# Performance work log

Hardware: AMD Instinct MI355X
Metric: run time of the kernel (lower is better)

Reference implementation:

```python
import jax, jax.numpy as jnp
import numpy as np

LN_EPS = 1e-5


def _layer_norm(x, scale, bias):
    mu = jnp.mean(x, axis=-1, keepdims=True)
    var = jnp.mean(jnp.square(x - mu), axis=-1, keepdims=True)
    return (x - mu) * jax.lax.rsqrt(var + LN_EPS) * scale + bias


def setup_inputs() -> dict:
    key = jax.random.key(0)
    B, N, C_Z, C_H = 1, 512, 128, 128
    ks = jax.random.split(key, 8)
    s = 1.0 / np.sqrt(C_Z)
    inp = {
        "z": jax.random.normal(ks[0], (B, N, N, C_Z), dtype=jnp.float32),
        "mask": jnp.ones((B, N, N), dtype=jnp.float32),
        # gated / plain projections from c_z -> c_hidden
        "w_a_p": jax.random.normal(ks[1], (C_Z, C_H), dtype=jnp.float32) * s,
        "b_a_p": jnp.zeros((C_H,), dtype=jnp.float32),
        "w_a_g": jnp.zeros((C_Z, C_H), dtype=jnp.float32),  # gating init: zeros, bias ones
        "b_a_g": jnp.ones((C_H,), dtype=jnp.float32),
        "w_b_p": jax.random.normal(ks[2], (C_Z, C_H), dtype=jnp.float32) * s,
        "b_b_p": jnp.zeros((C_H,), dtype=jnp.float32),
        "w_b_g": jnp.zeros((C_Z, C_H), dtype=jnp.float32),
        "b_b_g": jnp.ones((C_H,), dtype=jnp.float32),
        # output gate c_z -> c_z (gating init)
        "w_g": jnp.zeros((C_Z, C_Z), dtype=jnp.float32),
        "b_g": jnp.ones((C_Z,), dtype=jnp.float32),
        # final projection c_hidden -> c_z ('final' init: zeros; use small randn for a nontrivial test)
        "w_z": jax.random.normal(ks[3], (C_H, C_Z), dtype=jnp.float32) * (1.0 / np.sqrt(C_H)),
        "b_z": jnp.zeros((C_Z,), dtype=jnp.float32),
        "ln_in_scale": jnp.ones((C_Z,), dtype=jnp.float32),
        "ln_in_bias": jnp.zeros((C_Z,), dtype=jnp.float32),
        "ln_out_scale": jnp.ones((C_H,), dtype=jnp.float32),
        "ln_out_bias": jnp.zeros((C_H,), dtype=jnp.float32),
    }
    return inp


def reference(z, mask, w_a_p, b_a_p, w_a_g, b_a_g, w_b_p, b_b_p, w_b_g, b_b_g,
              w_g, b_g, w_z, b_z, ln_in_scale, ln_in_bias, ln_out_scale, ln_out_bias):
    # tmu_type == 'outgoing'
    z = _layer_norm(z, ln_in_scale, ln_in_bias)          # [B,N,N,Cz]
    m = mask[..., None]                                   # [B,N,N,1]
    a = jax.nn.sigmoid(z @ w_a_g + b_a_g) * m * (z @ w_a_p + b_a_p)  # [B,N,N,Ch]
    b = jax.nn.sigmoid(z @ w_b_g + b_b_g) * m * (z @ w_b_p + b_b_p)  # [B,N,N,Ch]
    # outgoing: p[b,i,j,c] = sum_k a[b,i,k,c] * b[b,j,k,c]
    x = jnp.einsum("bikc,bjkc->bijc", a, b)              # [B,N,N,Ch]
    x = _layer_norm(x, ln_out_scale, ln_out_bias)
    x = x @ w_z + b_z                                    # [B,N,N,Cz]
    g = jax.nn.sigmoid(z @ w_g + b_g)                    # [B,N,N,Cz]
    return x * g
```

## Files before the change

kernel.cpp:

```cpp
#include <hip/hip_runtime.h>

typedef __attribute__((ext_vector_type(8))) short short8;
typedef __attribute__((ext_vector_type(4))) short short4v;
typedef __attribute__((ext_vector_type(4))) float float4v;
typedef __attribute__((ext_vector_type(2))) unsigned int uint2v;

#define NDIM 512
#define NN (NDIM*NDIM)
#define CD 128

__device__ __forceinline__ unsigned short f2b(float f) {
  union { float f; unsigned u; } v; v.f = f;
  unsigned r = v.u + 0x7FFFu + ((v.u >> 16) & 1u);
  return (unsigned short)(r >> 16);
}
__device__ __forceinline__ float b2f(unsigned short h) {
  union { unsigned u; float f; } v; v.u = ((unsigned)h) << 16; return v.f;
}
__device__ __forceinline__ float sigmoidf_(float x) { return 1.f / (1.f + __expf(-x)); }
__device__ __forceinline__ unsigned pk2(float a, float b) {
  return (unsigned)f2b(a) | ((unsigned)f2b(b) << 16);
}
__device__ __forceinline__ float4v mfma16(short8 a, short8 b, float4v c) {
  return __builtin_amdgcn_mfma_f32_16x16x32_bf16(a, b, c, 0, 0, 0);
}
__device__ __forceinline__ void gl_lds16(const short* g, short* l) {
  __builtin_amdgcn_global_load_lds(
      (const __attribute__((address_space(1))) unsigned int*)g,
      (__attribute__((address_space(3))) unsigned int*)l, 16, 0, 0);
}

__device__ __forceinline__ short8 fragr(const short* buf, int row, int j) {
  return *(const short8*)(buf + row * 128 + ((j ^ (row & 15)) << 3));
}

__device__ __forceinline__ void stageW(const short* wslot, short* sW, int t) {
#pragma unroll
  for (int i = 0; i < 8; ++i) {
    int U = i * 256 + t;
    int row = U >> 4, u = U & 15;
    gl_lds16(wslot + row * 128 + ((u ^ (row & 15)) << 3), sW + U * 8);
  }
}

__global__ __launch_bounds__(256) void kPrepW(
    const float* __restrict__ w0, const float* __restrict__ w1,
    const float* __restrict__ w2, const float* __restrict__ w3,
    const float* __restrict__ w4, short* __restrict__ wt)
{
  const int wi = blockIdx.y;
  const float* W = wi==0 ? w0 : wi==1 ? w1 : wi==2 ? w2 : wi==3 ? w3 : w4;
  const int e = blockIdx.x * 256 + threadIdx.x;
  const int k = e >> 7, n = e & 127;
  wt[wi * 16384 + n * 128 + k] = (short)f2b(W[k * CD + n]);
}

__global__ __launch_bounds__(256, 2) void kProj(
    const float* __restrict__ z, const float* __restrict__ mask,
    const short* __restrict__ wT,
    const float* __restrict__ b_a_p, const float* __restrict__ b_a_g,
    const float* __restrict__ b_b_p, const float* __restrict__ b_b_g,
    const float* __restrict__ b_g,
    const float* __restrict__ ln_s, const float* __restrict__ ln_b,
    short* __restrict__ a_t, short* __restrict__ b_t, short* __restrict__ g_out)
{
  __shared__ short zln[128 * 128];
  __shared__ short sW[128 * 128];
  const int t = threadIdx.x;
  const int r0 = blockIdx.x * 128;
  const int w = t >> 6, l = t & 63, lr = l & 15, lg = l >> 4;

  stageW(wT + 1 * 16384, sW, t);

#pragma unroll
  for (int h = 0; h < 2; ++h) {
    const int row = h * 64 + (t >> 2), q = t & 3;
    const float* zp = z + (size_t)(r0 + row) * CD + q * 32;
    float x[32];
#pragma unroll
    for (int i = 0; i < 8; ++i) {
      float4v v = *(const float4v*)(zp + i * 4);
#pragma unroll
      for (int e = 0; e < 4; ++e) x[i*4+e] = v[e];
    }
    float s = 0.f;
#pragma unroll
    for (int i = 0; i < 32; ++i) s += x[i];
    s += __shfl_xor(s, 1, 64);
    s += __shfl_xor(s, 2, 64);
    const float mu = s * (1.f/128.f);
    float vs = 0.f;
#pragma unroll
    for (int i = 0; i < 32; ++i) { float d = x[i]-mu; vs += d*d; }
    vs += __shfl_xor(vs, 1, 64);
    vs += __shfl_xor(vs, 2, 64);
    const float rstd = rsqrtf(vs * (1.f/128.f) + 1e-5f);
#pragma unroll
    for (int i = 0; i < 32; ++i) {
      int c = q*32 + i;
      float y = (x[i]-mu)*rstd*ln_s[c] + ln_b[c];
      zln[row*128 + (((c>>3) ^ (row & 15)) << 3) + (c & 7)] = (short)f2b(y);
    }
  }

  float bga[8], bpa[8], bgb[8], bpb[8];
#pragma unroll
  for (int cf = 0; cf < 8; ++cf) {
    bga[cf] = b_a_g[cf*16+lr]; bpa[cf] = b_a_p[cf*16+lr];
    bgb[cf] = b_b_g[cf*16+lr]; bpb[cf] = b_b_p[cf*16+lr];
  }
  float mrow[2][4];
#pragma unroll
  for (int g = 0; g < 2; ++g)
#pragma unroll
    for (int jj = 0; jj < 4; ++jj)
      mrow[g][jj] = mask[r0 + w*32 + g*16 + lg*4 + jj];

  __syncthreads();

  short8 af[2][4];
#pragma unroll
  for (int g = 0; g < 2; ++g)
#pragma unroll
    for (int ks = 0; ks < 4; ++ks)
      af[g][ks] = fragr(zln, w*32 + g*16 + lr, ks*4 + lg);

  float4v accA[2][8], accB[2][8];
  float sg[2][8][4];

#define ZERO_ACC(A) do { _Pragma("unroll") for (int g_=0;g_<2;++g_) \
  _Pragma("unroll") for (int c_=0;c_<8;++c_) A[g_][c_] = (float4v){0.f,0.f,0.f,0.f}; } while(0)

#define WPASS(A) do { ZERO_ACC(A);                                         \
  _Pragma("unroll") for (int ks_=0; ks_<4; ++ks_)                          \
    _Pragma("unroll") for (int cf_=0; cf_<8; ++cf_) {                      \
      short8 wf_ = fragr(sW, cf_*16 + lr, ks_*4 + lg);                     \
      _Pragma("unroll") for (int g_=0; g_<2; ++g_)                         \
        A[g_][cf_] = mfma16(af[g_][ks_], wf_, A[g_][cf_]);                 \
    } } while(0)

#define SIGPASS(BG) do { _Pragma("unroll") for (int g_=0;g_<2;++g_)        \
  _Pragma("unroll") for (int cf_=0;cf_<8;++cf_)                            \
    _Pragma("unroll") for (int j_=0;j_<4;++j_)                             \
      sg[g_][cf_][j_] = sigmoidf_(accA[g_][cf_][j_] + BG[cf_]) * mrow[g_][j_]; } while(0)

#define STORE_AB(DST, BP) do { _Pragma("unroll") for (int g_=0;g_<2;++g_)  \
  _Pragma("unroll") for (int cf_=0;cf_<8;++cf_) {                          \
    float v0_ = sg[g_][cf_][0] * (accB[g_][cf_][0] + BP[cf_]);             \
    float v1_ = sg[g_][cf_][1] * (accB[g_][cf_][1] + BP[cf_]);             \
    float v2_ = sg[g_][cf_][2] * (accB[g_][cf_][2] + BP[cf_]);             \
    float v3_ = sg[g_][cf_][3] * (accB[g_][cf_][3] + BP[cf_]);             \
    uint2v pv_ = { pk2(v0_, v1_), pk2(v2_, v3_) };                         \
    *(uint2v*)(DST + (size_t)(cf_*16+lr)*NN + r0 + w*32 + g_*16 + lg*4) = pv_; \
  } } while(0)

  WPASS(accA);
  SIGPASS(bga);
  __syncthreads();
  stageW(wT + 0 * 16384, sW, t);
  __syncthreads();
  WPASS(accB);
  __syncthreads();
  stageW(wT + 3 * 16384, sW, t);
  STORE_AB(a_t, bpa);
  __syncthreads();
  WPASS(accA);
  SIGPASS(bgb);
  __syncthreads();
  stageW(wT + 2 * 16384, sW, t);
  __syncthreads();
  WPASS(accB);
  __syncthreads();
  stageW(wT + 4 * 16384, sW, t);
  STORE_AB(b_t, bpb);
  __syncthreads();
  {
    float4v accG[2][8];
    ZERO_ACC(accG);
#pragma unroll
    for (int ks = 0; ks < 4; ++ks)
#pragma unroll
      for (int cf = 0; cf < 8; ++cf) {
        short8 wf = fragr(sW, cf*16 + lr, ks*4 + lg);
#pragma unroll
        for (int g = 0; g < 2; ++g)
          accG[g][cf] = mfma16(wf, af[g][ks], accG[g][cf]);
      }
#pragma unroll
    for (int g = 0; g < 2; ++g)
#pragma unroll
      for (int cf = 0; cf < 8; ++cf) {
        float4v bgv = *(const float4v*)(b_g + cf*16 + lg*4);
        float v0 = sigmoidf_(accG[g][cf][0] + bgv[0]);
        float v1 = sigmoidf_(accG[g][cf][1] + bgv[1]);
        float v2 = sigmoidf_(accG[g][cf][2] + bgv[2]);
        float v3 = sigmoidf_(accG[g][cf][3] + bgv[3]);
        uint2v pv = { pk2(v0, v1), pk2(v2, v3) };
        *(uint2v*)(g_out + (size_t)(r0 + w*32 + g*16 + lr)*CD + cf*16 + lg*4) = pv;
      }
  }
}

__global__ __launch_bounds__(256, 2) void kEinsum(const short* __restrict__ a_t,
                                                  const short* __restrict__ b_t,
                                                  short* __restrict__ x_t)
{
  __shared__ short As[2][128 * 64];
  __shared__ short Bs[2][128 * 64];
  const int t = threadIdx.x;
  const int d = blockIdx.x;
  const int c = (d & 7) * 16 + (d >> 7);
  const int tile = (d >> 3) & 15;
  const int i0 = (tile >> 2) * 128;
  const int j0 = (tile & 3) * 128;
  const size_t abase = (size_t)c * NN;
  const int w = t >> 6, l = t & 63, lr = l & 15, lg = l >> 4;
  const int wr = w >> 1, wc = w & 1;

  const short* gA[4]; const short* gB[4]; int ldsU[4];
#pragma unroll
  for (int q = 0; q < 4; ++q) {
    int U = q * 256 + t;
    int row = U >> 3, u = U & 7;
    int swz = ((u ^ (row & 7)) << 3);
    gA[q] = a_t + abase + (size_t)(i0 + row) * NDIM + swz;
    gB[q] = b_t + abase + (size_t)(j0 + row) * NDIM + swz;
    ldsU[q] = U * 8;
  }

#define STAGE_E(buf, k0) do { _Pragma("unroll") for (int q_=0;q_<4;++q_) { \
    gl_lds16(gA[q_] + (k0), &As[buf][ldsU[q_]]);                           \
    gl_lds16(gB[q_] + (k0), &Bs[buf][ldsU[q_]]); } } while(0)

  float4v acc[4][4];
#pragma unroll
  for (int m = 0; m < 4; ++m)
#pragma unroll
    for (int n = 0; n < 4; ++n) acc[m][n] = (float4v){0.f,0.f,0.f,0.f};

  STAGE_E(0, 0);
  __syncthreads();
  int cur = 0;
#pragma unroll
  for (int it = 0; it < 8; ++it) {
    if (it < 7) STAGE_E(cur ^ 1, (it + 1) * 64);
    short8 afr[4][2], bfr[4][2];
#pragma unroll
    for (int m = 0; m < 4; ++m)
#pragma unroll
      for (int ks = 0; ks < 2; ++ks) {
        int row = wr*64 + m*16 + lr, j = ks*4 + lg;
        afr[m][ks] = *(const short8*)(&As[cur][row*64 + ((j ^ (row & 7)) << 3)]);
      }
#pragma unroll
    for (int n = 0; n < 4; ++n)
#pragma unroll
      for (int ks = 0; ks < 2; ++ks) {
        int row = wc*64 + n*16 + lr, j = ks*4 + lg;
        bfr[n][ks] = *(const short8*)(&Bs[cur][row*64 + ((j ^ (row & 7)) << 3)]);
      }
#pragma unroll
    for (int ks = 0; ks < 2; ++ks)
#pragma unroll
      for (int m = 0; m < 4; ++m)
#pragma unroll
        for (int n = 0; n < 4; ++n)
          acc[m][n] = mfma16(bfr[n][ks], afr[m][ks], acc[m][n]);
    __syncthreads();
    cur ^= 1;
  }
#pragma unroll
  for (int m = 0; m < 4; ++m)
#pragma unroll
    for (int n = 0; n < 4; ++n) {
      int i  = i0 + wr*64 + m*16 + lr;
      int jb = j0 + wc*64 + n*16 + lg*4;
      uint2v pv = { pk2(acc[m][n][0], acc[m][n][1]), pk2(acc[m][n][2], acc[m][n][3]) };
      *(uint2v*)(x_t + abase + (size_t)i * NDIM + jb) = pv;
    }
}

__global__ __launch_bounds__(256, 2) void kOut(
    const short* __restrict__ x_t, const short* __restrict__ g_in,
    const float* __restrict__ w_z, const float* __restrict__ b_z,
    const float* __restrict__ ln_s, const float* __restrict__ ln_b,
    float* __restrict__ out)
{
  __shared__ short xs[128 * 72];
  __shared__ short xln[64 * 128];
  __shared__ short sW[128 * 128];
  const int t = threadIdx.x;
  const int r0 = blockIdx.x * 64;
  const int w = t >> 6, l = t & 63, lr = l & 15, lg = l >> 4;

#pragma unroll
  for (int i = 0; i < 8; ++i) {
    int flat = i * 256 + t;
    int kp = flat >> 5, k = kp * 2, n4 = (flat & 31) * 4;
    float4v va = *(const float4v*)(w_z + (size_t)k * CD + n4);
    float4v vb = *(const float4v*)(w_z + (size_t)(k + 1) * CD + n4);
#pragma unroll
    for (int j = 0; j < 4; ++j) {
      int row = n4 + j;
      int addr = row * 128 + (((k >> 3) ^ (row & 15)) << 3) + (k & 7);
      *(unsigned*)(&sW[addr]) = pk2(va[j], vb[j]);
    }
  }
#pragma unroll
  for (int it = 0; it < 4; ++it) {
    int v = it * 256 + t; int cc = v >> 3; int u = v & 7;
    int up = u ^ ((cc >> 3) & 7);
    *(short8*)&xs[cc * 72 + up * 8] = *(const short8*)(x_t + (size_t)cc * NN + r0 + u * 8);
  }
  __syncthreads();
  {
    const int r = t >> 2, q = t & 3;
    float x[32];
#pragma unroll
    for (int i = 0; i < 32; ++i) {
      int c = q * 32 + i;
      x[i] = b2f((unsigned short)xs[c * 72 + (((r >> 3) ^ ((c >> 3) & 7)) << 3) + (r & 7)]);
    }
    float s = 0.f;
#pragma unroll
    for (int i = 0; i < 32; ++i) s += x[i];
    s += __shfl_xor(s, 1, 64);
    s += __shfl_xor(s, 2, 64);
    const float mu = s * (1.f/128.f);
    float vs = 0.f;
#pragma unroll
    for (int i = 0; i < 32; ++i) { float d = x[i]-mu; vs += d*d; }
    vs += __shfl_xor(vs, 1, 64);
    vs += __shfl_xor(vs, 2, 64);
    const float rstd = rsqrtf(vs * (1.f/128.f) + 1e-5f);
#pragma unroll
    for (int i = 0; i < 32; ++i) {
      int c = q*32 + i;
      float y = (x[i]-mu)*rstd*ln_s[c] + ln_b[c];
      xln[r*128 + (((c>>3) ^ (r & 15)) << 3) + (c & 7)] = (short)f2b(y);
    }
  }
  __syncthreads();
  short8 af[4];
#pragma unroll
  for (int ks = 0; ks < 4; ++ks)
    af[ks] = fragr(xln, w*16 + lr, ks*4 + lg);

  float4v acc[8];
#pragma unroll
  for (int cf = 0; cf < 8; ++cf) acc[cf] = (float4v){0.f,0.f,0.f,0.f};
#pragma unroll
  for (int ks = 0; ks < 4; ++ks)
#pragma unroll
    for (int cf = 0; cf < 8; ++cf) {
      short8 wf = fragr(sW, cf*16 + lr, ks*4 + lg);
      acc[cf] = mfma16(wf, af[ks], acc[cf]);
    }
  const int orow = r0 + w*16 + lr;
#pragma unroll
  for (int cf = 0; cf < 8; ++cf) {
    float4v bzv = *(const float4v*)(b_z + cf*16 + lg*4);
    short4v gv = *(const short4v*)(g_in + (size_t)orow * CD + cf*16 + lg*4);
    float4v o;
#pragma unroll
    for (int j = 0; j < 4; ++j)
      o[j] = (acc[cf][j] + bzv[j]) * b2f((unsigned short)gv[j]);
    *(float4v*)(out + (size_t)orow * CD + cf*16 + lg*4) = o;
  }
}

extern "C" void kernel_launch(void* const* d_in, const int* in_sizes, int n_in,
                              void* d_out, int out_size, void* d_ws, size_t ws_size,
                              hipStream_t stream) {
  (void)in_sizes; (void)n_in; (void)out_size; (void)ws_size;
  const float* z     = (const float*)d_in[0];
  const float* mask  = (const float*)d_in[1];
  const float* w_a_p = (const float*)d_in[2];
  const float* b_a_p = (const float*)d_in[3];
  const float* w_a_g = (const float*)d_in[4];
  const float* b_a_g = (const float*)d_in[5];
  const float* w_b_p = (const float*)d_in[6];
  const float* b_b_p = (const float*)d_in[7];
  const float* w_b_g = (const float*)d_in[8];
  const float* b_b_g = (const float*)d_in[9];
  const float* w_g   = (const float*)d_in[10];
  const float* b_g   = (const float*)d_in[11];
  const float* w_z   = (const float*)d_in[12];
  const float* b_z   = (const float*)d_in[13];
  const float* ln_i_s = (const float*)d_in[14];
  const float* ln_i_b = (const float*)d_in[15];
  const float* ln_o_s = (const float*)d_in[16];
  const float* ln_o_b = (const float*)d_in[17];

  short* a_t = (short*)d_ws;
  short* b_t = a_t + (size_t)CD*NN;
  short* g_s = b_t + (size_t)CD*NN;
  short* x_t = g_s + (size_t)CD*NN;
  short* wT  = x_t;

  hipLaunchKernelGGL(kPrepW, dim3(64, 5), dim3(256), 0, stream,
                     w_a_p, w_a_g, w_b_p, w_b_g, w_g, wT);
  hipLaunchKernelGGL(kProj, dim3(NN/128), dim3(256), 0, stream,
                     z, mask, wT, b_a_p, b_a_g, b_b_p, b_b_g, b_g,
                     ln_i_s, ln_i_b, a_t, b_t, g_s);
  hipLaunchKernelGGL(kEinsum, dim3(2048), dim3(256), 0, stream, a_t, b_t, x_t);
  hipLaunchKernelGGL(kOut, dim3(NN/64), dim3(256), 0, stream,
                     x_t, g_s, w_z, b_z, ln_o_s, ln_o_b, (float*)d_out);
}
```

Measured before the change: 366.0 us.

## Restructure projection kernel and stage all epilogue stores through LDS for coalescing

The projection kernel moves to 512 threads over 64 rows with double weight buffers, so gate and projection weights are staged together and fewer barriers are needed. Its channel-major a/b outputs and the g output are now written through shared memory as 16-byte coalesced stores. The einsum and output kernels also stage their epilogues through swizzled LDS before wide global stores. The einsum gains s_setprio around its MFMA block, and bf16 packing now uses a v_cvt_pk_bf16_f32 instruction. The gain is aimed at scattered narrow global writes, paid for with more LDS use and extra barriers that may reduce occupancy.

```diff
diff --git a/kernel.cpp b/kernel.cpp
--- a/kernel.cpp
+++ b/kernel.cpp
@@ -3,7 +3,6 @@
 typedef __attribute__((ext_vector_type(8))) short short8;
 typedef __attribute__((ext_vector_type(4))) short short4v;
 typedef __attribute__((ext_vector_type(4))) float float4v;
-typedef __attribute__((ext_vector_type(2))) unsigned int uint2v;
 
 #define NDIM 512
 #define NN (NDIM*NDIM)
@@ -19,7 +18,9 @@
 }
 __device__ __forceinline__ float sigmoidf_(float x) { return 1.f / (1.f + __expf(-x)); }
 __device__ __forceinline__ unsigned pk2(float a, float b) {
-  return (unsigned)f2b(a) | ((unsigned)f2b(b) << 16);
+  unsigned r;
+  asm("v_cvt_pk_bf16_f32 %0, %1, %2" : "=v"(r) : "v"(a), "v"(b));
+  return r;
 }
 __device__ __forceinline__ float4v mfma16(short8 a, short8 b, float4v c) {
   return __builtin_amdgcn_mfma_f32_16x16x32_bf16(a, b, c, 0, 0, 0);
@@ -33,14 +34,8 @@
 __device__ __forceinline__ short8 fragr(const short* buf, int row, int j) {
   return *(const short8*)(buf + row * 128 + ((j ^ (row & 15)) << 3));
 }
-
-__device__ __forceinline__ void stageW(const short* wslot, short* sW, int t) {
-#pragma unroll
-  for (int i = 0; i < 8; ++i) {
-    int U = i * 256 + t;
-    int row = U >> 4, u = U & 15;
-    gl_lds16(wslot + row * 128 + ((u ^ (row & 15)) << 3), sW + U * 8);
-  }
+__device__ __forceinline__ void stg_w(short* buf, int row, int ku, unsigned v) {
+  *(unsigned*)&buf[row * 128 + ((((ku >> 2) ^ (row & 15)) << 3) + ((ku & 3) << 1))] = v;
 }
 
 __global__ __launch_bounds__(256) void kPrepW(
@@ -55,7 +50,7 @@
   wt[wi * 16384 + n * 128 + k] = (short)f2b(W[k * CD + n]);
 }
 
-__global__ __launch_bounds__(256, 2) void kProj(
+__global__ __launch_bounds__(512, 2) void kProj(
     const float* __restrict__ z, const float* __restrict__ mask,
     const short* __restrict__ wT,
     const float* __restrict__ b_a_p, const float* __restrict__ b_a_g,
@@ -64,140 +59,158 @@
     const float* __restrict__ ln_s, const float* __restrict__ ln_b,
     short* __restrict__ a_t, short* __restrict__ b_t, short* __restrict__ g_out)
 {
-  __shared__ short zln[128 * 128];
-  __shared__ short sW[128 * 128];
+  __shared__ short zln[64 * 128];
+  __shared__ short sS[128 * 128];
+  __shared__ short wA[128 * 128];
+  __shared__ short wB[128 * 128];
   const int t = threadIdx.x;
-  const int r0 = blockIdx.x * 128;
+  const int r0 = blockIdx.x * 64;
   const int w = t >> 6, l = t & 63, lr = l & 15, lg = l >> 4;
-
-  stageW(wT + 1 * 16384, sW, t);
-
-#pragma unroll
-  for (int h = 0; h < 2; ++h) {
-    const int row = h * 64 + (t >> 2), q = t & 3;
-    const float* zp = z + (size_t)(r0 + row) * CD + q * 32;
-    float x[32];
-#pragma unroll
-    for (int i = 0; i < 8; ++i) {
+  const int wr = (w >> 1) * 16;
+  const int hc = (w & 1) * 64;
+
+#define STAGE4(BUF, SLOT) do { _Pragma("unroll") for (int i_=0;i_<4;++i_) {  \
+    int U_ = i_*512 + t; int row_ = U_ >> 4, u_ = U_ & 15;                   \
+    gl_lds16(wT + (SLOT)*16384 + row_*128 + ((u_^(row_&15))<<3), (BUF)+U_*8); } } while(0)
+
+  STAGE4(wA, 1);
+  STAGE4(wB, 0);
+
+  {
+    const int row = t >> 3, q = t & 7;
+    const float* zp = z + (size_t)(r0 + row) * CD + q * 16;
+    float x[16];
+#pragma unroll
+    for (int i = 0; i < 4; ++i) {
       float4v v = *(const float4v*)(zp + i * 4);
 #pragma unroll
       for (int e = 0; e < 4; ++e) x[i*4+e] = v[e];
     }
     float s = 0.f;
 #pragma unroll
-    for (int i = 0; i < 32; ++i) s += x[i];
+    for (int i = 0; i < 16; ++i) s += x[i];
     s += __shfl_xor(s, 1, 64);
     s += __shfl_xor(s, 2, 64);
+    s += __shfl_xor(s, 4, 64);
     const float mu = s * (1.f/128.f);
     float vs = 0.f;
 #pragma unroll
-    for (int i = 0; i < 32; ++i) { float d = x[i]-mu; vs += d*d; }
+    for (int i = 0; i < 16; ++i) { float d = x[i]-mu; vs += d*d; }
     vs += __shfl_xor(vs, 1, 64);
     vs += __shfl_xor(vs, 2, 64);
+    vs += __shfl_xor(vs, 4, 64);
     const float rstd = rsqrtf(vs * (1.f/128.f) + 1e-5f);
 #pragma unroll
-    for (int i = 0; i < 32; ++i) {
-      int c = q*32 + i;
-      float y = (x[i]-mu)*rstd*ln_s[c] + ln_b[c];
-      zln[row*128 + (((c>>3) ^ (row & 15)) << 3) + (c & 7)] = (short)f2b(y);
-    }
-  }
-
-  float bga[8], bpa[8], bgb[8], bpb[8];
-#pragma unroll
-  for (int cf = 0; cf < 8; ++cf) {
-    bga[cf] = b_a_g[cf*16+lr]; bpa[cf] = b_a_p[cf*16+lr];
-    bgb[cf] = b_b_g[cf*16+lr]; bpb[cf] = b_b_p[cf*16+lr];
-  }
-  float mrow[2][4];
-#pragma unroll
-  for (int g = 0; g < 2; ++g)
-#pragma unroll
-    for (int jj = 0; jj < 4; ++jj)
-      mrow[g][jj] = mask[r0 + w*32 + g*16 + lg*4 + jj];
-
-  __syncthreads();
-
-  short8 af[2][4];
-#pragma unroll
-  for (int g = 0; g < 2; ++g)
+    for (int i = 0; i < 16; i += 2) {
+      int c = q*16 + i;
+      float y0 = (x[i]  -mu)*rstd*ln_s[c]   + ln_b[c];
+      float y1 = (x[i+1]-mu)*rstd*ln_s[c+1] + ln_b[c+1];
+      int addr = row*128 + (((c>>3) ^ (row & 15)) << 3) + (c & 7);
+      *(unsigned*)(&zln[addr]) = pk2(y0, y1);
+    }
+  }
+
+  float bga[4], bpa[4], bgb[4], bpb[4];
+#pragma unroll
+  for (int cf = 0; cf < 4; ++cf) {
+    int ci = hc + cf*16 + lr;
+    bga[cf] = b_a_g[ci]; bpa[cf] = b_a_p[ci];
+    bgb[cf] = b_b_g[ci]; bpb[cf] = b_b_p[ci];
+  }
+  float mrow[4];
+#pragma unroll
+  for (int jj = 0; jj < 4; ++jj) mrow[jj] = mask[r0 + wr + lg*4 + jj];
+
+  __syncthreads();
+
+  short8 af[4];
+#pragma unroll
+  for (int ks = 0; ks < 4; ++ks)
+    af[ks] = fragr(zln, wr + lr, ks*4 + lg);
+
+  float4v accG[4], accB[4];
+  float sg[4][4];
+
+#define ZERO4(A) do { _Pragma("unroll") for (int c_=0;c_<4;++c_) A[c_] = (float4v){0.f,0.f,0.f,0.f}; } while(0)
+
+#define WP(ACC, BUF) do { ZERO4(ACC);                                      \
+  _Pragma("unroll") for (int ks_=0; ks_<4; ++ks_)                          \
+    _Pragma("unroll") for (int cf_=0; cf_<4; ++cf_) {                      \
+      short8 wf_ = fragr(BUF, hc + cf_*16 + lr, ks_*4 + lg);               \
+      ACC[cf_] = mfma16(af[ks_], wf_, ACC[cf_]);                           \
+    } } while(0)
+
+#define SIG4(BG) do { _Pragma("unroll") for (int cf_=0;cf_<4;++cf_)        \
+    _Pragma("unroll") for (int j_=0;j_<4;++j_)                             \
+      sg[cf_][j_] = sigmoidf_(accG[cf_][j_] + BG[cf_]) * mrow[j_]; } while(0)
+
+#define PKAB(BP) do { _Pragma("unroll") for (int cf_=0;cf_<4;++cf_) {      \
+    float v0_ = sg[cf_][0]*(accB[cf_][0]+BP[cf_]);                         \
+    float v1_ = sg[cf_][1]*(accB[cf_][1]+BP[cf_]);                         \
+    float v2_ = sg[cf_][2]*(accB[cf_][2]+BP[cf_]);                         \
+    float v3_ = sg[cf_][3]*(accB[cf_][3]+BP[cf_]);                         \
+    int ch_ = hc + cf_*16 + lr, ku_ = (wr >> 1) + lg*2;                    \
+    stg_w(sS, ch_, ku_,   pk2(v0_, v1_));                                  \
+    stg_w(sS, ch_, ku_+1, pk2(v2_, v3_)); } } while(0)
+
+#define STORE64A(DST) do { int ch_ = t >> 2;                               \
+  _Pragma("unroll") for (int i_=0;i_<2;++i_) {                             \
+    int cL_ = (t & 3)*2 + i_;                                              \
+    *(short8*)(DST + (size_t)ch_*NN + r0 + cL_*8) = fragr(sS, ch_, cL_);   \
+  } } while(0)
+
+  WP(accG, wA);
+  WP(accB, wB);
+  SIG4(bga);
+  PKAB(bpa);
+  __syncthreads();
+
+  STAGE4(wA, 3);
+  STAGE4(wB, 2);
+  STORE64A(a_t);
+  __syncthreads();
+
+  WP(accG, wA);
+  WP(accB, wB);
+  SIG4(bgb);
+  PKAB(bpb);
+  __syncthreads();
+
+  STAGE4(wA, 4);
+  STORE64A(b_t);
+  __syncthreads();
+
+  {
+    float4v accG2[4];
+    ZERO4(accG2);
 #pragma unroll
     for (int ks = 0; ks < 4; ++ks)
-      af[g][ks] = fragr(zln, w*32 + g*16 + lr, ks*4 + lg);
-
-  float4v accA[2][8], accB[2][8];
-  float sg[2][8][4];
-
-#define ZERO_ACC(A) do { _Pragma("unroll") for (int g_=0;g_<2;++g_) \
-  _Pragma("unroll") for (int c_=0;c_<8;++c_) A[g_][c_] = (float4v){0.f,0.f,0.f,0.f}; } while(0)
-
-#define WPASS(A) do { ZERO_ACC(A);                                         \
-  _Pragma("unroll") for (int ks_=0; ks_<4; ++ks_)                          \
-    _Pragma("unroll") for (int cf_=0; cf_<8; ++cf_) {                      \
-      short8 wf_ = fragr(sW, cf_*16 + lr, ks_*4 + lg);                     \
-      _Pragma("unroll") for (int g_=0; g_<2; ++g_)                         \
-        A[g_][cf_] = mfma16(af[g_][ks_], wf_, A[g_][cf_]);                 \
-    } } while(0)
-
-#define SIGPASS(BG) do { _Pragma("unroll") for (int g_=0;g_<2;++g_)        \
-  _Pragma("unroll") for (int cf_=0;cf_<8;++cf_)                            \
-    _Pragma("unroll") for (int j_=0;j_<4;++j_)                             \
-      sg[g_][cf_][j_] = sigmoidf_(accA[g_][cf_][j_] + BG[cf_]) * mrow[g_][j_]; } while(0)
-
-#define STORE_AB(DST, BP) do { _Pragma("unroll") for (int g_=0;g_<2;++g_)  \
-  _Pragma("unroll") for (int cf_=0;cf_<8;++cf_) {                          \
-    float v0_ = sg[g_][cf_][0] * (accB[g_][cf_][0] + BP[cf_]);             \
-    float v1_ = sg[g_][cf_][1] * (accB[g_][cf_][1] + BP[cf_]);             \
-    float v2_ = sg[g_][cf_][2] * (accB[g_][cf_][2] + BP[cf_]);             \
-    float v3_ = sg[g_][cf_][3] * (accB[g_][cf_][3] + BP[cf_]);             \
-    uint2v pv_ = { pk2(v0_, v1_), pk2(v2_, v3_) };                         \
-    *(uint2v*)(DST + (size_t)(cf_*16+lr)*NN + r0 + w*32 + g_*16 + lg*4) = pv_; \
-  } } while(0)
-
-  WPASS(accA);
-  SIGPASS(bga);
-  __syncthreads();
-  stageW(wT + 0 * 16384, sW, t);
-  __syncthreads();
-  WPASS(accB);
-  __syncthreads();
-  stageW(wT + 3 * 16384, sW, t);
-  STORE_AB(a_t, bpa);
-  __syncthreads();
-  WPASS(accA);
-  SIGPASS(bgb);
-  __syncthreads();
-  stageW(wT + 2 * 16384, sW, t);
-  __syncthreads();
-  WPASS(accB);
-  __syncthreads();
-  stageW(wT + 4 * 16384, sW, t);
-  STORE_AB(b_t, bpb);
-  __syncthreads();
+#pragma unroll
+      for (int cf = 0; cf < 4; ++cf) {
+        short8 wf = fragr(wA, hc + cf*16 + lr, ks*4 + lg);
+        accG2[cf] = mfma16(wf, af[ks], accG2[cf]);
+      }
+#pragma unroll
+    for (int cf = 0; cf < 4; ++cf) {
+      float4v bgv = *(const float4v*)(b_g + hc + cf*16 + lg*4);
+      float v0 = sigmoidf_(accG2[cf][0] + bgv[0]);
+      float v1 = sigmoidf_(accG2[cf][1] + bgv[1]);
+      float v2 = sigmoidf_(accG2[cf][2] + bgv[2]);
+      float v3 = sigmoidf_(accG2[cf][3] + bgv[3]);
+      int row = wr + lr, ku = (hc >> 1) + cf*8 + lg*2;
+      stg_w(sS, row, ku,   pk2(v0, v1));
+      stg_w(sS, row, ku+1, pk2(v2, v3));
+    }
+  }
+  __syncthreads();
+
   {
-    float4v accG[2][8];
-    ZERO_ACC(accG);
-#pragma unroll
-    for (int ks = 0; ks < 4; ++ks)
-#pragma unroll
-      for (int cf = 0; cf < 8; ++cf) {
-        short8 wf = fragr(sW, cf*16 + lr, ks*4 + lg);
-#pragma unroll
-        for (int g = 0; g < 2; ++g)
-          accG[g][cf] = mfma16(wf, af[g][ks], accG[g][cf]);
-      }
-#pragma unroll
-    for (int g = 0; g < 2; ++g)
-#pragma unroll
-      for (int cf = 0; cf < 8; ++cf) {
-        float4v bgv = *(const float4v*)(b_g + cf*16 + lg*4);
-        float v0 = sigmoidf_(accG[g][cf][0] + bgv[0]);
-        float v1 = sigmoidf_(accG[g][cf][1] + bgv[1]);
-        float v2 = sigmoidf_(accG[g][cf][2] + bgv[2]);
-        float v3 = sigmoidf_(accG[g][cf][3] + bgv[3]);
-        uint2v pv = { pk2(v0, v1), pk2(v2, v3) };
-        *(uint2v*)(g_out + (size_t)(r0 + w*32 + g*16 + lr)*CD + cf*16 + lg*4) = pv;
-      }
+    int row = t >> 3;
+#pragma unroll
+    for (int i = 0; i < 2; ++i) {
+      int cL = (t & 7)*2 + i;
+      *(short8*)(g_out + (size_t)(r0 + row)*CD + cL*8) = fragr(sS, row, cL);
+    }
   }
 }
 
@@ -259,6 +272,7 @@
         int row = wc*64 + n*16 + lr, j = ks*4 + lg;
         bfr[n][ks] = *(const short8*)(&Bs[cur][row*64 + ((j ^ (row & 7)) << 3)]);
       }
+    __builtin_amdgcn_s_setprio(1);
 #pragma unroll
     for (int ks = 0; ks < 2; ++ks)
 #pragma unroll
@@ -266,18 +280,26 @@
 #pragma unroll
         for (int n = 0; n < 4; ++n)
           acc[m][n] = mfma16(bfr[n][ks], afr[m][ks], acc[m][n]);
+    __builtin_amdgcn_s_setprio(0);
     __syncthreads();
     cur ^= 1;
   }
+  short* Xs = &As[0][0];
 #pragma unroll
   for (int m = 0; m < 4; ++m)
 #pragma unroll
     for (int n = 0; n < 4; ++n) {
-      int i  = i0 + wr*64 + m*16 + lr;
-      int jb = j0 + wc*64 + n*16 + lg*4;
-      uint2v pv = { pk2(acc[m][n][0], acc[m][n][1]), pk2(acc[m][n][2], acc[m][n][3]) };
-      *(uint2v*)(x_t + abase + (size_t)i * NDIM + jb) = pv;
-    }
+      int il = wr*64 + m*16 + lr;
+      int ku = wc*32 + n*8 + lg*2;
+      stg_w(Xs, il, ku,   pk2(acc[m][n][0], acc[m][n][1]));
+      stg_w(Xs, il, ku+1, pk2(acc[m][n][2], acc[m][n][3]));
+    }
+  __syncthreads();
+#pragma unroll
+  for (int i = 0; i < 8; ++i) {
+    int il = t >> 1, cL = (t & 1)*8 + i;
+    *(short8*)(x_t + abase + (size_t)(i0 + il)*NDIM + j0 + cL*8) = fragr(Xs, il, cL);
+  }
 }
 
 __global__ __launch_bounds__(256, 2) void kOut(
@@ -356,7 +378,10 @@
       short8 wf = fragr(sW, cf*16 + lr, ks*4 + lg);
       acc[cf] = mfma16(wf, af[ks], acc[cf]);
     }
+  __syncthreads();
+  float* fWs = (float*)sW;
   const int orow = r0 + w*16 + lr;
+  const int rl = w*16 + lr;
 #pragma unroll
   for (int cf = 0; cf < 8; ++cf) {
     float4v bzv = *(const float4v*)(b_z + cf*16 + lg*4);
@@ -365,7 +390,14 @@
 #pragma unroll
     for (int j = 0; j < 4; ++j)
       o[j] = (acc[cf][j] + bzv[j]) * b2f((unsigned short)gv[j]);
-    *(float4v*)(out + (size_t)orow * CD + cf*16 + lg*4) = o;
+    *(float4v*)&fWs[rl*128 + (((cf*4+lg) ^ (rl & 15)) << 2)] = o;
+  }
+  __syncthreads();
+#pragma unroll
+  for (int i = 0; i < 8; ++i) {
+    int row = t >> 2, cL = (t & 3)*8 + i;
+    *(float4v*)(out + (size_t)(r0 + row)*CD + cL*4) =
+        *(const float4v*)&fWs[row*128 + ((cL ^ (row & 15)) << 2)];
   }
 }
 
@@ -400,7 +432,7 @@
 
   hipLaunchKernelGGL(kPrepW, dim3(64, 5), dim3(256), 0, stream,
                      w_a_p, w_a_g, w_b_p, w_b_g, w_g, wT);
-  hipLaunchKernelGGL(kProj, dim3(NN/128), dim3(256), 0, stream,
+  hipLaunchKernelGGL(kProj, dim3(NN/64), dim3(512), 0, stream,
                      z, mask, wT, b_a_p, b_a_g, b_b_p, b_b_g, b_g,
                      ln_i_s, ln_i_b, a_t, b_t, g_s);
   hipLaunchKernelGGL(kEinsum, dim3(2048), dim3(256), 0, stream, a_t, b_t, x_t);
```

After: 362.6 us. No clear change (-0.9%).
